# Performance work log

Measured on AMD Instinct MI355X. Metric: run time of the kernel, lower is better.

## Reference

```python
import jax, jax.numpy as jnp
import numpy as np

NUM_MODALS = 4
SHARED_IDX = 3  # forward always uses adapter index 3 as the shared LoRA

def setup_inputs() -> dict:
    key = jax.random.key(0)
    k1, k2, k3, k4, k5 = jax.random.split(key, 5)
    M, B, n, c, r = NUM_MODALS, 8, 1024, 768, 16
    x = jax.random.normal(k1, (M * B, n, c), dtype=jnp.float32)
    Wp = jax.random.normal(k2, (c, c), dtype=jnp.float32) * 0.02   # proj weight [out,in]
    bp = jax.random.normal(k3, (c,), dtype=jnp.float32) * 0.02     # proj bias
    A = jax.random.normal(k4, (M, r, c), dtype=jnp.float32) * 0.02  # linear_a_o weights [r,c]
    Bw = jax.random.normal(k5, (M, c, r), dtype=jnp.float32) * 0.02 # linear_b_o weights [c,r]
    return {"x": x, "Wp": Wp, "bp": bp, "A": A, "Bw": Bw}

def reference(x, Wp, bp, A, Bw):
    bs_m, n, c = x.shape
    xm = x.reshape(NUM_MODALS, -1, n, c)  # [M,B,n,c]
    # base projection (dense GEMM) + bias
    base = jnp.einsum('mbnc,oc->mbno', xm, Wp) + bp
    # shared LoRA (adapter index 3 for every modality)
    sh_lo = jnp.einsum('mbnc,rc->mbnr', xm, A[SHARED_IDX])
    shared = jnp.einsum('mbnr,or->mbno', sh_lo, Bw[SHARED_IDX])
    # modality-specific LoRA (batched over modality axis)
    sp_lo = jnp.einsum('mbnc,mrc->mbnr', xm, A)
    specific = jnp.einsum('mbnr,mor->mbno', sp_lo, Bw)
    out = base + shared + specific
    return out.reshape(bs_m, n, -1)
```

## Files before the change

kernel.cpp:

```cpp
#include <hip/hip_runtime.h>
#include <hip/hip_bf16.h>
#include <stdint.h>

#define NUM_MODALS 4
#define SHARED_IDX 3

typedef __attribute__((ext_vector_type(8))) short bf16x8;
typedef __attribute__((ext_vector_type(4))) float floatx4;

__device__ __forceinline__ unsigned short f2bf(float f) {
  unsigned int u = __float_as_uint(f);
  u += 0x7fffu + ((u >> 16) & 1u);
  return (unsigned short)(u >> 16);
}

__global__ __launch_bounds__(256) void weff_fast(
    const float* __restrict__ Wp, const float* __restrict__ A,
    const float* __restrict__ Bw, unsigned short* __restrict__ Weff) {
  const int c  = blockIdx.x * 256 + threadIdx.x;
  const int o0 = blockIdx.y * 16;
  const int m  = blockIdx.z;

  __shared__ float b3[256], bm[256];
  const int t = threadIdx.x;
  {
    const int o = o0 + (t >> 4);
    const int r = t & 15;
    b3[t] = Bw[(SHARED_IDX * 768 + o) * 16 + r];
    bm[t] = Bw[((size_t)m * 768 + o) * 16 + r];
  }
  __syncthreads();

  float a3[16], am[16];
#pragma unroll
  for (int r = 0; r < 16; ++r) {
    a3[r] = A[(SHARED_IDX * 16 + r) * 768 + c];
    am[r] = A[((size_t)m * 16 + r) * 768 + c];
  }
#pragma unroll 4
  for (int oo = 0; oo < 16; ++oo) {
    const int o = o0 + oo;
    float acc = Wp[(size_t)o * 768 + c];
#pragma unroll
    for (int r = 0; r < 16; ++r) {
      acc += b3[oo * 16 + r] * a3[r];
      acc += bm[oo * 16 + r] * am[r];
    }
    Weff[((size_t)m * 768 + o) * 768 + c] = f2bf(acc);
  }
}

__global__ __launch_bounds__(256) void lora_gemm_fused(
    const float* __restrict__ X,
    const unsigned short* __restrict__ Weff,
    const float* __restrict__ bp,
    float* __restrict__ out) {
  const int bid = blockIdx.x;
  const int xcd = bid & 7;
  const int s   = bid >> 3;
  const int w   = xcd * 192 + s;
  const int ct  = w % 6;
  const int rt  = w / 6;
  const int m        = rt >> 6;
  const int row_base = (rt & 63) * 128;
  const int col_base = ct * 128;

  __shared__ alignas(16) unsigned short As[128 * 64];
  __shared__ alignas(16) unsigned short Ws[2 * 128 * 64];

  const int tid  = threadIdx.x;
  const int wave = tid >> 6;
  const int lane = tid & 63;
  const int ln = lane & 15;
  const int qd = lane >> 4;
  const int wm = wave & 1;
  const int wn = wave >> 1;

  const float*          Xm = X    + (size_t)m * 8192 * 768;
  const unsigned short* Wm = Weff + (size_t)m * 768 * 768;

  floatx4 acc[4][4];
#pragma unroll
  for (int i = 0; i < 4; ++i)
#pragma unroll
    for (int j = 0; j < 4; ++j)
      acc[i][j] = (floatx4)(0.0f);

  const int xr   = tid >> 4;
  const int xc   = (tid & 15) * 4;
  const int cb   = xc >> 3;
  const int half = (xc >> 2) & 1;
  const float* xsrc[8];
  unsigned short* xdst[8];
#pragma unroll
  for (int p = 0; p < 8; ++p) {
    const int r = xr + p * 16;
    xsrc[p] = Xm + (size_t)(row_base + r) * 768 + xc;
    xdst[p] = &As[r * 64 + (cb ^ (r & 7)) * 8 + half * 4];
  }
  const int sr = lane >> 3;
  const int ss = lane & 7;
  const unsigned short* wsrc[4];
#pragma unroll
  for (int p = 0; p < 4; ++p) {
    const int r = wave * 32 + p * 8 + sr;
    wsrc[p] = Wm + (size_t)(col_base + r) * 768 + (ss ^ (r & 7)) * 8;
  }

  float4 xv[8];
#pragma unroll
  for (int p = 0; p < 4; ++p) {
    __builtin_amdgcn_global_load_lds(
        (const __attribute__((address_space(1))) void*)wsrc[p],
        (__attribute__((address_space(3))) void*)&Ws[(wave * 32 + p * 8) * 64],
        16, 0, 0);
    wsrc[p] += 64;
  }
#pragma unroll
  for (int p = 0; p < 8; ++p) {
    xv[p] = *(const float4*)xsrc[p];
    xsrc[p] += 64;
  }
#pragma unroll
  for (int p = 0; p < 4; ++p) {
    __builtin_amdgcn_global_load_lds(
        (const __attribute__((address_space(1))) void*)wsrc[p],
        (__attribute__((address_space(3))) void*)&Ws[128 * 64 + (wave * 32 + p * 8) * 64],
        16, 0, 0);
    wsrc[p] += 64;
  }

  for (int kt = 0; kt < 12; ++kt) {
    const int boff = (kt & 1) * (128 * 64);

    if (kt < 11) {
      asm volatile("s_waitcnt vmcnt(4)" ::: "memory");
    } else {
      asm volatile("s_waitcnt vmcnt(0)" ::: "memory");
    }

#pragma unroll
    for (int p = 0; p < 8; ++p) {
      const float4 v = xv[p];
      __hip_bfloat162 h0 = __float22bfloat162_rn(make_float2(v.x, v.y));
      __hip_bfloat162 h1 = __float22bfloat162_rn(make_float2(v.z, v.w));
      uint2 hv;
      hv.x = *(unsigned int*)&h0;
      hv.y = *(unsigned int*)&h1;
      *(uint2*)xdst[p] = hv;
    }

    if (kt < 11) {
#pragma unroll
      for (int p = 0; p < 8; ++p) {
        xv[p] = *(const float4*)xsrc[p];
        xsrc[p] += 64;
      }
    }

    asm volatile("s_waitcnt lgkmcnt(0)" ::: "memory");
    __builtin_amdgcn_sched_barrier(0);
    __builtin_amdgcn_s_barrier();
    __builtin_amdgcn_sched_barrier(0);

    __builtin_amdgcn_s_setprio(1);
#pragma unroll
    for (int kk = 0; kk < 64; kk += 32) {
      const int kblk = (kk >> 3) + qd;
      const int slot = (kblk ^ (ln & 7)) * 8;
      bf16x8 a[4], b[4];
#pragma unroll
      for (int i = 0; i < 4; ++i)
        a[i] = *(const bf16x8*)(&As[(wm * 64 + i * 16 + ln) * 64 + slot]);
#pragma unroll
      for (int j = 0; j < 4; ++j)
        b[j] = *(const bf16x8*)(&Ws[boff + (wn * 64 + j * 16 + ln) * 64 + slot]);
#pragma unroll
      for (int i = 0; i < 4; ++i)
#pragma unroll
        for (int j = 0; j < 4; ++j)
          acc[i][j] = __builtin_amdgcn_mfma_f32_16x16x32_bf16(a[i], b[j], acc[i][j], 0, 0, 0);
    }
    __builtin_amdgcn_s_setprio(0);

    __builtin_amdgcn_sched_barrier(0);
    __builtin_amdgcn_s_barrier();
    __builtin_amdgcn_sched_barrier(0);

    if (kt < 10) {
#pragma unroll
      for (int p = 0; p < 4; ++p) {
        __builtin_amdgcn_global_load_lds(
            (const __attribute__((address_space(1))) void*)wsrc[p],
            (__attribute__((address_space(3))) void*)&Ws[boff + (wave * 32 + p * 8) * 64],
            16, 0, 0);
        wsrc[p] += 64;
      }
    }
  }

  float* Om = out + (size_t)m * 8192 * 768;
#pragma unroll
  for (int j = 0; j < 4; ++j) {
    const int o = col_base + wn * 64 + j * 16 + ln;
    const float bias = bp[o];
#pragma unroll
    for (int i = 0; i < 4; ++i) {
      const int R = row_base + wm * 64 + i * 16 + qd * 4;
      float* dst = Om + (size_t)R * 768 + o;
#pragma unroll
      for (int v = 0; v < 4; ++v)
        dst[(size_t)v * 768] = acc[i][j][v] + bias;
    }
  }
}

extern "C" void kernel_launch(void* const* d_in, const int* in_sizes, int n_in,
                              void* d_out, int out_size, void* d_ws, size_t ws_size,
                              hipStream_t stream) {
  const float* x  = (const float*)d_in[0];
  const float* Wp = (const float*)d_in[1];
  const float* bp = (const float*)d_in[2];
  const float* A  = (const float*)d_in[3];
  const float* Bw = (const float*)d_in[4];
  float* out = (float*)d_out;

  unsigned short* Weff = (unsigned short*)d_ws;

  weff_fast<<<dim3(3, 48, 4), 256, 0, stream>>>(Wp, A, Bw, Weff);
  lora_gemm_fused<<<dim3(1536), 256, 0, stream>>>(x, Weff, bp, out);
}
```

Before: 232.6 us.

## Deepen X prefetch to two register stages and unroll K loop by two

The main K loop is unrolled by two so that X tiles are double-buffered in registers (xv[2][8]). Each fp32 tile is loaded two K-steps before it is converted and stored to LDS, and the waits are relaxed to vmcnt(12) so more global loads stay in flight. Launch bounds now request 3 blocks per CU to limit register growth. The extra 32 float registers per thread add register pressure, and the occupancy hint may force spills.

```diff
diff --git a/kernel.cpp b/kernel.cpp
--- a/kernel.cpp
+++ b/kernel.cpp
@@ -50,7 +50,7 @@
   }
 }
 
-__global__ __launch_bounds__(256) void lora_gemm_fused(
+__global__ __launch_bounds__(256, 3) void lora_gemm_fused(
     const float* __restrict__ X,
     const unsigned short* __restrict__ Weff,
     const float* __restrict__ bp,
@@ -107,7 +107,7 @@
     wsrc[p] = Wm + (size_t)(col_base + r) * 768 + (ss ^ (r & 7)) * 8;
   }
 
-  float4 xv[8];
+  float4 xv[2][8];
 #pragma unroll
   for (int p = 0; p < 4; ++p) {
     __builtin_amdgcn_global_load_lds(
@@ -118,7 +118,7 @@
   }
 #pragma unroll
   for (int p = 0; p < 8; ++p) {
-    xv[p] = *(const float4*)xsrc[p];
+    xv[0][p] = *(const float4*)xsrc[p];
     xsrc[p] += 64;
   }
 #pragma unroll
@@ -129,19 +129,19 @@
         16, 0, 0);
     wsrc[p] += 64;
   }
-
-  for (int kt = 0; kt < 12; ++kt) {
-    const int boff = (kt & 1) * (128 * 64);
-
-    if (kt < 11) {
-      asm volatile("s_waitcnt vmcnt(4)" ::: "memory");
-    } else {
-      asm volatile("s_waitcnt vmcnt(0)" ::: "memory");
-    }
-
+#pragma unroll
+  for (int p = 0; p < 8; ++p) {
+    xv[1][p] = *(const float4*)xsrc[p];
+    xsrc[p] += 64;
+  }
+
+  for (int kt2 = 0; kt2 < 6; ++kt2) {
+    const bool pf = (kt2 < 5);
+
+    asm volatile("s_waitcnt vmcnt(12)" ::: "memory");
 #pragma unroll
     for (int p = 0; p < 8; ++p) {
-      const float4 v = xv[p];
+      const float4 v = xv[0][p];
       __hip_bfloat162 h0 = __float22bfloat162_rn(make_float2(v.x, v.y));
       __hip_bfloat162 h1 = __float22bfloat162_rn(make_float2(v.z, v.w));
       uint2 hv;
@@ -149,15 +149,13 @@
       hv.y = *(unsigned int*)&h1;
       *(uint2*)xdst[p] = hv;
     }
-
-    if (kt < 11) {
+    if (pf) {
 #pragma unroll
       for (int p = 0; p < 8; ++p) {
-        xv[p] = *(const float4*)xsrc[p];
+        xv[0][p] = *(const float4*)xsrc[p];
         xsrc[p] += 64;
       }
     }
-
     asm volatile("s_waitcnt lgkmcnt(0)" ::: "memory");
     __builtin_amdgcn_sched_barrier(0);
     __builtin_amdgcn_s_barrier();
@@ -174,7 +172,7 @@
         a[i] = *(const bf16x8*)(&As[(wm * 64 + i * 16 + ln) * 64 + slot]);
 #pragma unroll
       for (int j = 0; j < 4; ++j)
-        b[j] = *(const bf16x8*)(&Ws[boff + (wn * 64 + j * 16 + ln) * 64 + slot]);
+        b[j] = *(const bf16x8*)(&Ws[(wn * 64 + j * 16 + ln) * 64 + slot]);
 #pragma unroll
       for (int i = 0; i < 4; ++i)
 #pragma unroll
@@ -187,12 +185,74 @@
     __builtin_amdgcn_s_barrier();
     __builtin_amdgcn_sched_barrier(0);
 
-    if (kt < 10) {
+    if (pf) {
 #pragma unroll
       for (int p = 0; p < 4; ++p) {
         __builtin_amdgcn_global_load_lds(
             (const __attribute__((address_space(1))) void*)wsrc[p],
-            (__attribute__((address_space(3))) void*)&Ws[boff + (wave * 32 + p * 8) * 64],
+            (__attribute__((address_space(3))) void*)&Ws[(wave * 32 + p * 8) * 64],
+            16, 0, 0);
+        wsrc[p] += 64;
+      }
+    }
+
+    if (pf) {
+      asm volatile("s_waitcnt vmcnt(12)" ::: "memory");
+    } else {
+      asm volatile("s_waitcnt vmcnt(0)" ::: "memory");
+    }
+#pragma unroll
+    for (int p = 0; p < 8; ++p) {
+      const float4 v = xv[1][p];
+      __hip_bfloat162 h0 = __float22bfloat162_rn(make_float2(v.x, v.y));
+      __hip_bfloat162 h1 = __float22bfloat162_rn(make_float2(v.z, v.w));
+      uint2 hv;
+      hv.x = *(unsigned int*)&h0;
+      hv.y = *(unsigned int*)&h1;
+      *(uint2*)xdst[p] = hv;
+    }
+    if (pf) {
+#pragma unroll
+      for (int p = 0; p < 8; ++p) {
+        xv[1][p] = *(const float4*)xsrc[p];
+        xsrc[p] += 64;
+      }
+    }
+    asm volatile("s_waitcnt lgkmcnt(0)" ::: "memory");
+    __builtin_amdgcn_sched_barrier(0);
+    __builtin_amdgcn_s_barrier();
+    __builtin_amdgcn_sched_barrier(0);
+
+    __builtin_amdgcn_s_setprio(1);
+#pragma unroll
+    for (int kk = 0; kk < 64; kk += 32) {
+      const int kblk = (kk >> 3) + qd;
+      const int slot = (kblk ^ (ln & 7)) * 8;
+      bf16x8 a[4], b[4];
+#pragma unroll
+      for (int i = 0; i < 4; ++i)
+        a[i] = *(const bf16x8*)(&As[(wm * 64 + i * 16 + ln) * 64 + slot]);
+#pragma unroll
+      for (int j = 0; j < 4; ++j)
+        b[j] = *(const bf16x8*)(&Ws[128 * 64 + (wn * 64 + j * 16 + ln) * 64 + slot]);
+#pragma unroll
+      for (int i = 0; i < 4; ++i)
+#pragma unroll
+        for (int j = 0; j < 4; ++j)
+          acc[i][j] = __builtin_amdgcn_mfma_f32_16x16x32_bf16(a[i], b[j], acc[i][j], 0, 0, 0);
+    }
+    __builtin_amdgcn_s_setprio(0);
+
+    __builtin_amdgcn_sched_barrier(0);
+    __builtin_amdgcn_s_barrier();
+    __builtin_amdgcn_sched_barrier(0);
+
+    if (pf) {
+#pragma unroll
+      for (int p = 0; p < 4; ++p) {
+        __builtin_amdgcn_global_load_lds(
+            (const __attribute__((address_space(1))) void*)wsrc[p],
+            (__attribute__((address_space(3))) void*)&Ws[128 * 64 + (wave * 32 + p * 8) * 64],
             16, 0, 0);
         wsrc[p] += 64;
       }
```

Result: slower. 455.5 us (+95.8%).
